# Kernel optimization log

Measured on AMD Instinct MI355X. Metric: run time of the kernel, lower is better.

The kernel has to match this reference:

```python
import jax, jax.numpy as jnp
import numpy as np

# Interpretation constants (external PersistentHomology class unavailable):
# each sample's feature vector is a point cloud of N_POINTS points in R^POINT_DIM.
N_POINTS = 1024
POINT_DIM = 128
WEIGHT = 1.0
N_TARGET_DIMS = 2  # target_dimensions = [0, 1]; H1 diagram is empty -> contributes 0


def _h0_mean_persistence(pts):
    """Exact H0 persistence of the Vietoris-Rips filtration of a point cloud.

    H0 pairs are (birth=0, death=w_e) for each edge w_e of the Euclidean MST,
    so persistence values are exactly the MST edge lengths (Prim's algorithm,
    vectorized over points, sequential over the N-1 tree-growth steps).
    pts: [N, d] -> scalar mean persistence.
    """
    n = pts.shape[0]
    mindist0 = jnp.linalg.norm(pts - pts[0], axis=-1)          # [N]
    visited0 = jnp.zeros((n,), dtype=bool).at[0].set(True)

    def step(carry, _):
        mindist, visited = carry
        masked = jnp.where(visited, jnp.inf, mindist)          # [N]
        j = jnp.argmin(masked)
        death = masked[j]                                      # MST edge length
        visited = visited.at[j].set(True)
        newd = jnp.linalg.norm(pts - pts[j], axis=-1)          # [N]
        mindist = jnp.minimum(mindist, newd)
        return (mindist, visited), death

    (_, _), deaths = jax.lax.scan(step, (mindist0, visited0), None, length=n - 1)
    return jnp.mean(deaths)


def setup_inputs() -> dict:
    key = jax.random.key(0)
    representations = jax.random.normal(key, (128, N_POINTS * POINT_DIM), dtype=jnp.float32)
    return {"representations": representations}


def reference(representations) -> jnp.ndarray:
    b = representations.shape[0]
    pts = representations.reshape(b, N_POINTS, POINT_DIM)      # per-sample point cloud
    per_sample = jax.vmap(_h0_mean_persistence)(pts)           # [B] mean H0 persistence
    # original: sum over batch and target dims (H1 empty), / (B * n_dims), * weight
    loss = jnp.sum(per_sample) / (b * N_TARGET_DIMS)
    return WEIGHT * loss
```

## Files before the change

kernel.cpp:

```cpp
#include <hip/hip_runtime.h>

typedef unsigned int uint_t;
typedef unsigned short ushort_t;
typedef unsigned char uchar_t;
typedef _Float16 h2 __attribute__((ext_vector_type(2)));
typedef _Float16 f16x8 __attribute__((ext_vector_type(8)));
typedef float f32x4 __attribute__((ext_vector_type(4)));

#define NPTS 1024
#define DIM  128
#define NH2  64

__device__ __forceinline__ float dot2f(uint_t a, uint_t b, float c) {
#if __has_builtin(__builtin_amdgcn_fdot2)
    return __builtin_amdgcn_fdot2(__builtin_bit_cast(h2, a),
                                  __builtin_bit_cast(h2, b), c, false);
#else
    h2 ha = __builtin_bit_cast(h2, a);
    h2 hb = __builtin_bit_cast(h2, b);
    c += (float)ha[0] * (float)hb[0];
    c += (float)ha[1] * (float)hb[1];
    return c;
#endif
}

__device__ __forceinline__ uint_t umin_u(uint_t a, uint_t b) { return a < b ? a : b; }
__device__ __forceinline__ uint_t umax_u(uint_t a, uint_t b) { return a > b ? a : b; }
__device__ __forceinline__ uint_t pk_min_u16(uint_t a, uint_t b) {
    uint_t d; asm("v_pk_min_u16 %0, %1, %2" : "=v"(d) : "v"(a), "v"(b)); return d;
}
__device__ __forceinline__ uint_t pk_max_u16(uint_t a, uint_t b) {
    uint_t d; asm("v_pk_max_u16 %0, %1, %2" : "=v"(d) : "v"(a), "v"(b)); return d;
}

#define DPP_UMIN(x, ctrl)                                                       \
    x = umin_u(x, (uint_t)__builtin_amdgcn_update_dpp((int)(x), (int)(x),       \
                                                      (ctrl), 0xf, 0xf, false))
#define DPP_REDUCE(x)                                                           \
    do { DPP_UMIN(x, 0x111); DPP_UMIN(x, 0x112); DPP_UMIN(x, 0x114);            \
         DPP_UMIN(x, 0x118); DPP_UMIN(x, 0x142); DPP_UMIN(x, 0x143); } while (0)

#define SEL_LO 0x05020400u
#define SEL_HI 0x07020600u

__device__ __forceinline__ void gload16(const void* g, void* l) {
#if __has_builtin(__builtin_amdgcn_global_load_lds)
    __builtin_amdgcn_global_load_lds(
        (__attribute__((address_space(1))) void*)(g),
        (__attribute__((address_space(3))) void*)(l), 16, 0, 0);
#else
    *(uint4*)l = *(const uint4*)g;
#endif
}

__global__ __launch_bounds__(256)
void prep_kernel(const float* __restrict__ reps, ushort_t* __restrict__ P16,
                 float* __restrict__ norms) {
    const int t   = threadIdx.x;
    const int row = blockIdx.x * 16 + (t >> 4);
    const int kx  = (t & 15) * 8;
    const float* src = reps + (size_t)row * DIM + kx;
    float4 v0 = *(const float4*)src;
    float4 v1 = *(const float4*)(src + 4);
    _Float16 h[8] = {(_Float16)v0.x, (_Float16)v0.y, (_Float16)v0.z, (_Float16)v0.w,
                     (_Float16)v1.x, (_Float16)v1.y, (_Float16)v1.z, (_Float16)v1.w};
    float nrm = 0.f;
    uint_t pk[4];
#pragma unroll
    for (int i = 0; i < 4; ++i) {
        float a = (float)h[2 * i], b = (float)h[2 * i + 1];
        nrm += a * a + b * b;
        pk[i] = (uint_t)__builtin_bit_cast(ushort_t, h[2 * i]) |
                ((uint_t)__builtin_bit_cast(ushort_t, h[2 * i + 1]) << 16);
    }
    *(uint4*)(P16 + (size_t)row * DIM + kx) = make_uint4(pk[0], pk[1], pk[2], pk[3]);
#pragma unroll
    for (int m = 1; m <= 8; m <<= 1) nrm += __shfl_xor(nrm, m, 16);
    if ((t & 15) == 0) norms[row] = nrm;
}

__global__ __launch_bounds__(256)
void norms_kernel(const float* __restrict__ reps, float* __restrict__ norms) {
    const int t   = threadIdx.x;
    const int row = blockIdx.x * 16 + (t >> 4);
    const int kx  = (t & 15) * 8;
    const float* src = reps + (size_t)row * DIM + kx;
    float4 v0 = *(const float4*)src;
    float4 v1 = *(const float4*)(src + 4);
    float nrm = 0.f;
    {
        _Float16 h[8] = {(_Float16)v0.x, (_Float16)v0.y, (_Float16)v0.z, (_Float16)v0.w,
                         (_Float16)v1.x, (_Float16)v1.y, (_Float16)v1.z, (_Float16)v1.w};
#pragma unroll
        for (int i = 0; i < 8; ++i) { float a = (float)h[i]; nrm += a * a; }
    }
#pragma unroll
    for (int m = 1; m <= 8; m <<= 1) nrm += __shfl_xor(nrm, m, 16);
    if ((t & 15) == 0) norms[row] = nrm;
}

__device__ __forceinline__ int swz(int row, int seg) {
    return (row << 7) + (((seg ^ row) & 15) << 3);
}
__device__ __forceinline__ uint_t packh2(float a, float b) {
    h2 p; p[0] = (_Float16)a; p[1] = (_Float16)b;
    return __builtin_bit_cast(uint_t, p);
}

__device__ __forceinline__ void gram_core_epilogue(
        f32x4 acc[2][8], const float* nrmS, uchar_t* Ds,
        int ti, int tj, int lane, int w) {
    const int cj = lane & 15;
    const int r4 = (lane >> 4) * 4;
    float na[2][4], nb[8];
#pragma unroll
    for (int mt = 0; mt < 2; ++mt)
#pragma unroll
        for (int r = 0; r < 4; ++r)
            na[mt][r] = nrmS[ti * 128 + w * 32 + mt * 16 + r4 + r];
#pragma unroll
    for (int nt = 0; nt < 8; ++nt) nb[nt] = nrmS[tj * 128 + nt * 16 + cj];
#pragma unroll
    for (int mt = 0; mt < 2; ++mt)
#pragma unroll
        for (int nt = 0; nt < 8; ++nt) {
            const int gj = tj * 128 + nt * 16 + cj;
#pragma unroll
            for (int r = 0; r < 4; ++r) {
                const int gi = ti * 128 + w * 32 + mt * 16 + r4 + r;
                float d2 = fmaxf(na[mt][r] + nb[nt] - 2.f * acc[mt][nt][r], 0.f);
                uint_t q = (uint_t)(d2 * 0.5f + 0.5f);
                q = q > 255u ? 255u : q;
                Ds[((size_t)gi << 10) + gj] = (uchar_t)q;
            }
        }
}

__global__ __launch_bounds__(256, 2)
void gram16_kernel(const ushort_t* __restrict__ P16, const float* __restrict__ norms,
                   uchar_t* __restrict__ D8, int xcd_affine) {
    __shared__ ushort_t At[128 * 128];
    __shared__ ushort_t Bt[128 * 128];
    const int bid = blockIdx.x;
    int s, tile;
    if (xcd_affine) {
        const int x = bid & 7, k = bid >> 3;
        s    = x + ((k >> 6) << 3);
        tile = k & 63;
    } else {
        s    = bid >> 6;
        tile = bid & 63;
    }
    const int ti = tile >> 3, tj = tile & 7;
    const int t  = threadIdx.x, lane = t & 63, w = t >> 6;

    const ushort_t* Pa = P16 + (((size_t)s * NPTS + (size_t)ti * 128) << 7);
    const ushort_t* Pb = P16 + (((size_t)s * NPTS + (size_t)tj * 128) << 7);
#pragma unroll
    for (int i = 0; i < 8; ++i) {
        const int c   = t + i * 256;
        const int row = c >> 4;
        const int seg = (c ^ row) & 15;
        const size_t go = ((size_t)row << 7) + (size_t)seg * 8;
        gload16(Pa + go, &At[(size_t)c * 8]);
        gload16(Pb + go, &Bt[(size_t)c * 8]);
    }
    __syncthreads();

    f32x4 acc[2][8] = {};
    const int mrow = lane & 15;
    const int lg   = lane >> 4;
#pragma unroll
    for (int q = 0; q < 4; ++q) {
        const int seg = q * 4 + lg;
        f16x8 a0 = *(const f16x8*)&At[swz(w * 32 + mrow, seg)];
        f16x8 a1 = *(const f16x8*)&At[swz(w * 32 + 16 + mrow, seg)];
#pragma unroll
        for (int nt = 0; nt < 8; ++nt) {
            f16x8 b = *(const f16x8*)&Bt[swz(nt * 16 + mrow, seg)];
            acc[0][nt] = __builtin_amdgcn_mfma_f32_16x16x32_f16(a0, b, acc[0][nt], 0, 0, 0);
            acc[1][nt] = __builtin_amdgcn_mfma_f32_16x16x32_f16(a1, b, acc[1][nt], 0, 0, 0);
        }
    }
    gram_core_epilogue(acc, norms + (size_t)s * NPTS, D8 + ((size_t)s << 20),
                       ti, tj, lane, w);
}

__global__ __launch_bounds__(256, 2)
void gram_kernel(const float* __restrict__ reps, const float* __restrict__ norms,
                 uchar_t* __restrict__ D8, int s_base) {
    __shared__ ushort_t At[128 * 128];
    __shared__ ushort_t Bt[128 * 128];
    const int bid  = blockIdx.x;
    const int sl   = bid >> 6, tile = bid & 63, ti = tile >> 3, tj = tile & 7;
    const int s    = s_base + sl;
    const int t    = threadIdx.x, lane = t & 63, w = t >> 6;

    const float* Pa = reps + ((size_t)s * NPTS + (size_t)ti * 128) * DIM;
    const float* Pb = reps + ((size_t)s * NPTS + (size_t)tj * 128) * DIM;
#pragma unroll
    for (int i = 0; i < 8; ++i) {
        int c = t + i * 256, row = c >> 4, seg = c & 15;
        const float* pa = Pa + row * DIM + seg * 8;
        const float* pb = Pb + row * DIM + seg * 8;
        float4 a0 = *(const float4*)pa, a1 = *(const float4*)(pa + 4);
        float4 b0 = *(const float4*)pb, b1 = *(const float4*)(pb + 4);
        *(uint4*)&At[swz(row, seg)] = make_uint4(packh2(a0.x, a0.y), packh2(a0.z, a0.w),
                                                 packh2(a1.x, a1.y), packh2(a1.z, a1.w));
        *(uint4*)&Bt[swz(row, seg)] = make_uint4(packh2(b0.x, b0.y), packh2(b0.z, b0.w),
                                                 packh2(b1.x, b1.y), packh2(b1.z, b1.w));
    }
    __syncthreads();

    f32x4 acc[2][8] = {};
    const int mrow = lane & 15;
    const int lg   = lane >> 4;
#pragma unroll
    for (int q = 0; q < 4; ++q) {
        const int seg = q * 4 + lg;
        f16x8 a0 = *(const f16x8*)&At[swz(w * 32 + mrow, seg)];
        f16x8 a1 = *(const f16x8*)&At[swz(w * 32 + 16 + mrow, seg)];
#pragma unroll
        for (int nt = 0; nt < 8; ++nt) {
            f16x8 b = *(const f16x8*)&Bt[swz(nt * 16 + mrow, seg)];
            acc[0][nt] = __builtin_amdgcn_mfma_f32_16x16x32_f16(a0, b, acc[0][nt], 0, 0, 0);
            acc[1][nt] = __builtin_amdgcn_mfma_f32_16x16x32_f16(a1, b, acc[1][nt], 0, 0, 0);
        }
    }
    gram_core_epilogue(acc, norms + (size_t)s * NPTS, D8 + ((size_t)sl << 20),
                       ti, tj, lane, w);
}

__global__ __launch_bounds__(256)
void nn4_kernel(const uchar_t* __restrict__ D8, uint_t* __restrict__ NN4) {
    const int lane = threadIdx.x & 63;
    const int wv   = threadIdx.x >> 6;
    const int base = blockIdx.x * 64 + wv * 16;

    uint_t slotv[8];
#pragma unroll
    for (int m = 0; m < 8; ++m)
        slotv[m] = ((uint_t)(2 * m + 1) << 16) | (uint_t)(2 * m);

    uint4 rc = ((const uint4*)(D8 + ((size_t)base << 10)))[lane];
    for (int i = 0; i < 16; ++i) {
        const int row = base + i;
        uint4 rn = rc;
        if (i < 15)
            rn = ((const uint4*)(D8 + ((size_t)(row + 1) << 10)))[lane];

        uint_t md[8];
        md[0] = __builtin_amdgcn_perm(rc.x, slotv[0], SEL_LO);
        md[1] = __builtin_amdgcn_perm(rc.x, slotv[1], SEL_HI);
        md[2] = __builtin_amdgcn_perm(rc.y, slotv[2], SEL_LO);
        md[3] = __builtin_amdgcn_perm(rc.y, slotv[3], SEL_HI);
        md[4] = __builtin_amdgcn_perm(rc.z, slotv[4], SEL_LO);
        md[5] = __builtin_amdgcn_perm(rc.z, slotv[5], SEL_HI);
        md[6] = __builtin_amdgcn_perm(rc.w, slotv[6], SEL_LO);
        md[7] = __builtin_amdgcn_perm(rc.w, slotv[7], SEL_HI);
        {
            const int r_in = row & 1023;
            const bool win = (r_in >> 4) == lane;
            const uint_t s4 = (uint_t)(r_in & 15);
#pragma unroll
            for (int m = 0; m < 8; ++m) {
                uint_t h = (win && s4 == 2u * m)      ? 0x0000FFFFu
                         : (win && s4 == 2u * m + 1u) ? 0xFFFF0000u : 0u;
                md[m] |= h;
            }
        }
        uint_t out4[4];
#pragma unroll
        for (int k = 0; k < 4; ++k) {
            uint_t t0 = pk_min_u16(pk_min_u16(md[0], md[1]), pk_min_u16(md[2], md[3]));
            uint_t t1 = pk_min_u16(pk_min_u16(md[4], md[5]), pk_min_u16(md[6], md[7]));
            uint_t tt = pk_min_u16(t0, t1);
            uint_t v16 = umin_u(tt & 0xFFFFu, tt >> 16);
            uint_t key = ((v16 & 0xFF00u) << 2) | ((uint_t)lane << 4) | (v16 & 15u);
            DPP_REDUCE(key);
            uint_t g = (uint_t)__builtin_amdgcn_readlane((int)key, 63);
            out4[k] = g;
            if (k < 3) {
                const uint_t wl = (g >> 4) & 63u, ws = g & 15u;
                const bool win = (uint_t)lane == wl;
#pragma unroll
                for (int m = 0; m < 8; ++m) {
                    uint_t h = (win && ws == 2u * m)      ? 0x0000FFFFu
                             : (win && ws == 2u * m + 1u) ? 0xFFFF0000u : 0u;
                    md[m] |= h;
                }
            }
        }
        if (lane == 0)
            *(uint4*)(NN4 + (size_t)row * 4) = make_uint4(out4[0], out4[1],
                                                          out4[2], out4[3]);
        rc = rn;
    }
}

__global__ __launch_bounds__(1024)
void boruvka4_kernel(const uchar_t* __restrict__ D8, const uint_t* __restrict__ NN4,
                     float* __restrict__ out, float scale) {
    const int sl   = blockIdx.x;
    const int v    = threadIdx.x;
    const int lane = v & 63;
    const int wv   = v >> 6;
    const uchar_t* Dbase = D8 + ((size_t)sl << 20);

    __shared__ ushort_t root16[NPTS];
    __shared__ uint_t   best[NPTS];
    __shared__ ushort_t rq[64];
    __shared__ uint_t   rqn, ncomp_s;
    __shared__ float    fsum[16];

    uint4 nA = *(const uint4*)(NN4 + (((size_t)sl << 10) + (size_t)v) * 4);
    uint_t nn[4] = {nA.x, nA.y, nA.z, nA.w};

    root16[v] = (ushort_t)v;
    float acc = 0.f;
    __syncthreads();

    for (int round = 0; round < 48; ++round) {
        best[v] = 0xFFFFFFFFu;
        if (v == 0) { rqn = 0; ncomp_s = 0; }
        __syncthreads();

        const uint_t rv = root16[v];

        uint_t cand = 0xFFFFFFFFu;
#pragma unroll
        for (int k = 0; k < 4; ++k) {
            uint_t e = nn[k];
            uint_t j = e & 1023u;
            if (root16[j] != (ushort_t)rv) {
                uint_t q = e >> 10;
                uint_t a = umin_u((uint_t)v, j), b = umax_u((uint_t)v, j);
                cand = umin_u(cand, (q << 20) | (a << 10) | b);
            }
        }
        if (cand != 0xFFFFFFFFu) atomicMin(&best[rv], cand);
        __syncthreads();

        if (rv == (uint_t)v && best[v] == 0xFFFFFFFFu) {
            uint_t idx = atomicAdd(&rqn, 1u);
            if (idx < 64u) rq[idx] = (ushort_t)v;
        }
        __syncthreads();

        if (rqn != 0u) {
            const uint_t nq = umin_u(rqn, 64u);
            for (uint_t qi = (uint_t)wv; qi < nq; qi += 16) {
                const uint_t row = rq[qi];
                const uint_t rr  = root16[row];
                uint4 r = ((const uint4*)(Dbase + ((size_t)row << 10)))[lane];
                uint_t bl = 0xFFFFFFFFu;
                const uint_t base = (uint_t)lane * 16u;
#pragma unroll
                for (int k = 0; k < 16; ++k) {
                    uint_t j = base + (uint_t)k;
                    uint_t q = (k < 4  ? (r.x >> (8 * k))
                              : k < 8  ? (r.y >> (8 * (k - 4)))
                              : k < 12 ? (r.z >> (8 * (k - 8)))
                                       : (r.w >> (8 * (k - 12)))) & 0xFFu;
                    uint_t a = umin_u(row, j), b = umax_u(row, j);
                    if (root16[j] != (ushort_t)rr)
                        bl = umin_u(bl, (q << 20) | (a << 10) | b);
                }
                DPP_REDUCE(bl);
                uint_t g = (uint_t)__builtin_amdgcn_readlane((int)bl, 63);
                if (lane == 0 && g != 0xFFFFFFFFu) atomicMin(&best[rr], g);
            }
            __syncthreads();
        }

        bool hook = false;
        uint_t o = (uint_t)v;
        if (rv == (uint_t)v) {
            uint_t K = best[v];
            if (K != 0xFFFFFFFFu) {
                uint_t a = (K >> 10) & 1023u, b = K & 1023u, q = K >> 20;
                uint_t ra = root16[a], rb = root16[b];
                o = (ra == (uint_t)v) ? rb : ra;
                if (o < (uint_t)v) {
                    hook = true;
                    acc += sqrtf(2.0f * (float)q);
                }
            }
        }
        __syncthreads();
        if (hook) root16[v] = (ushort_t)o;
        __syncthreads();

        uint_t r = root16[v];
        uint_t pr = root16[r];
        for (int sg = 0; sg < 64 && pr != r; ++sg) { r = pr; pr = root16[r]; }
        __syncthreads();
        root16[v] = (ushort_t)r;

        unsigned long long ball = __ballot(r == (uint_t)v);
        if (lane == 0) atomicAdd(&ncomp_s, (uint_t)__popcll(ball));
        __syncthreads();
        if (ncomp_s == 1u) break;
    }

#pragma unroll
    for (int m = 32; m >= 1; m >>= 1) acc += __shfl_xor(acc, m, 64);
    if (lane == 0) fsum[wv] = acc;
    __syncthreads();
    if (v == 0) {
        float s = 0.f;
#pragma unroll
        for (int i = 0; i < 16; ++i) s += fsum[i];
        atomicAdd(out, s * scale);
    }
}

__global__ __launch_bounds__(1024)
void boruvka_kernel(const uchar_t* __restrict__ D8, float* __restrict__ out,
                    float scale) {
    const int sl   = blockIdx.x;
    const int v    = threadIdx.x;
    const int lane = v & 63;
    const int wv   = v >> 6;
    const uchar_t* Dbase = D8 + ((size_t)sl << 20);

    __shared__ uint_t   nnlist[NPTS * 8];
    __shared__ ushort_t root16[NPTS];
    __shared__ uint_t   best[NPTS];
    __shared__ ushort_t rq[NPTS];
    __shared__ uint_t   rqn, ncomp_s;
    __shared__ float    fsum[16];

    uint_t slotv[8];
#pragma unroll
    for (int m = 0; m < 8; ++m)
        slotv[m] = ((uint_t)(2 * m + 1) << 16) | (uint_t)(2 * m);

    {
        uint4 rc = ((const uint4*)(Dbase + ((size_t)wv << 10)))[lane];
        for (int i = 0; i < 64; ++i) {
            const int row = wv + 16 * i;
            uint4 rn = rc;
            if (i < 63)
                rn = ((const uint4*)(Dbase + ((size_t)(row + 16) << 10)))[lane];
            uint_t md[8];
            md[0] = __builtin_amdgcn_perm(rc.x, slotv[0], SEL_LO);
            md[1] = __builtin_amdgcn_perm(rc.x, slotv[1], SEL_HI);
            md[2] = __builtin_amdgcn_perm(rc.y, slotv[2], SEL_LO);
            md[3] = __builtin_amdgcn_perm(rc.y, slotv[3], SEL_HI);
            md[4] = __builtin_amdgcn_perm(rc.z, slotv[4], SEL_LO);
            md[5] = __builtin_amdgcn_perm(rc.z, slotv[5], SEL_HI);
            md[6] = __builtin_amdgcn_perm(rc.w, slotv[6], SEL_LO);
            md[7] = __builtin_amdgcn_perm(rc.w, slotv[7], SEL_HI);
            {
                const bool win = (row >> 4) == lane;
                const uint_t s4 = (uint_t)(row & 15);
#pragma unroll
                for (int m = 0; m < 8; ++m) {
                    uint_t h = (win && s4 == 2u * m)      ? 0x0000FFFFu
                             : (win && s4 == 2u * m + 1u) ? 0xFFFF0000u : 0u;
                    md[m] |= h;
                }
            }
#pragma unroll
            for (int k = 0; k < 8; ++k) {
                uint_t t0 = pk_min_u16(pk_min_u16(md[0], md[1]), pk_min_u16(md[2], md[3]));
                uint_t t1 = pk_min_u16(pk_min_u16(md[4], md[5]), pk_min_u16(md[6], md[7]));
                uint_t tt = pk_min_u16(t0, t1);
                uint_t v16 = umin_u(tt & 0xFFFFu, tt >> 16);
                uint_t key = ((v16 & 0xFF00u) << 2) | ((uint_t)lane << 4) | (v16 & 15u);
                DPP_REDUCE(key);
                uint_t g = (uint_t)__builtin_amdgcn_readlane((int)key, 63);
                if (lane == 0) nnlist[row * 8 + k] = g;
                const uint_t wl = (g >> 4) & 63u, ws = g & 15u;
                const bool win = (uint_t)lane == wl;
#pragma unroll
                for (int m = 0; m < 8; ++m) {
                    uint_t h = (win && ws == 2u * m)      ? 0x0000FFFFu
                             : (win && ws == 2u * m + 1u) ? 0xFFFF0000u : 0u;
                    md[m] |= h;
                }
            }
            rc = rn;
        }
    }
    root16[v] = (ushort_t)v;
    __syncthreads();

    uint_t nn[8];
#pragma unroll
    for (int k = 0; k < 8; ++k) nn[k] = nnlist[v * 8 + k];
    const uint_t q8 = nn[7] >> 10;

    float acc = 0.f;
    for (int round = 0; round < 12; ++round) {
        best[v] = 0xFFFFFFFFu;
        if (v == 0) { rqn = 0; ncomp_s = 0; }
        __syncthreads();
        const uint_t rv = root16[v];
        uint_t cand = 0xFFFFFFFFu;
#pragma unroll
        for (int k = 0; k < 8; ++k) {
            uint_t e = nn[k];
            uint_t j = e & 1023u;
            if (root16[j] != (ushort_t)rv) {
                uint_t q = e >> 10;
                uint_t a = umin_u((uint_t)v, j), b = umax_u((uint_t)v, j);
                cand = umin_u(cand, (q << 20) | (a << 10) | b);
            }
        }
        if (cand != 0xFFFFFFFFu) atomicMin(&best[rv], cand);
        if (cand == 0xFFFFFFFFu || (cand >> 20) >= q8) {
            uint_t idx = atomicAdd(&rqn, 1u);
            rq[idx] = (ushort_t)v;
        }
        __syncthreads();
        for (uint_t qi = (uint_t)wv; qi < rqn; qi += 16) {
            const uint_t row = rq[qi];
            const uint_t rr  = root16[row];
            uint4 r = ((const uint4*)(Dbase + ((size_t)row << 10)))[lane];
            uint_t bl = 0xFFFFFFFFu;
            const uint_t base = (uint_t)lane * 16u;
#pragma unroll
            for (int k = 0; k < 16; ++k) {
                uint_t j = base + (uint_t)k;
                uint_t q = (k < 4  ? (r.x >> (8 * k))
                          : k < 8  ? (r.y >> (8 * (k - 4)))
                          : k < 12 ? (r.z >> (8 * (k - 8)))
                                   : (r.w >> (8 * (k - 12)))) & 0xFFu;
                uint_t a = umin_u(row, j), b = umax_u(row, j);
                if (root16[j] != (ushort_t)rr)
                    bl = umin_u(bl, (q << 20) | (a << 10) | b);
            }
            DPP_REDUCE(bl);
            uint_t g = (uint_t)__builtin_amdgcn_readlane((int)bl, 63);
            if (lane == 0 && g != 0xFFFFFFFFu) atomicMin(&best[rr], g);
        }
        __syncthreads();
        const bool isroot = (rv == (uint_t)v);
        bool hook = false;
        uint_t o = (uint_t)v;
        if (isroot) {
            uint_t K = best[v];
            if (K != 0xFFFFFFFFu) {
                uint_t a = (K >> 10) & 1023u, b = K & 1023u, q = K >> 20;
                uint_t ra = root16[a], rb = root16[b];
                o = (ra == (uint_t)v) ? rb : ra;
                bool mutual = (best[o] == K);
                if (!mutual || (uint_t)v > o) {
                    hook = true;
                    acc += sqrtf(2.0f * (float)q);
                }
            }
        }
        __syncthreads();
        if (hook) root16[v] = (ushort_t)o;
        __syncthreads();
        uint_t r = root16[v];
        uint_t pr = root16[r];
        for (int sgs = 0; sgs < 1024 && pr != r; ++sgs) { r = pr; pr = root16[r]; }
        __syncthreads();
        root16[v] = (ushort_t)r;
        unsigned long long ball = __ballot(r == (uint_t)v);
        if (lane == 0) atomicAdd(&ncomp_s, (uint_t)__popcll(ball));
        __syncthreads();
        if (ncomp_s == 1u) break;
    }
#pragma unroll
    for (int m = 32; m >= 1; m >>= 1) acc += __shfl_xor(acc, m, 64);
    if (lane == 0) fsum[wv] = acc;
    __syncthreads();
    if (v == 0) {
        float s = 0.f;
#pragma unroll
        for (int i = 0; i < 16; ++i) s += fsum[i];
        atomicAdd(out, s * scale);
    }
}

__global__ __launch_bounds__(64, 1)
void prim_u8_kernel(const uchar_t* __restrict__ D8, float* __restrict__ out,
                    float scale) {
    const int sl   = blockIdx.x;
    const int lane = threadIdx.x;
    const uchar_t* Dbase = D8 + ((size_t)sl << 20);

    uint_t md[8], po[8], slotv[8];
#pragma unroll
    for (int m = 0; m < 8; ++m) {
        md[m] = 0xFFFFFFFFu; po[m] = 0u;
        slotv[m] = ((uint_t)(2 * m + 1) << 16) | (uint_t)(2 * m);
    }
    const uint_t lane16 = (uint_t)lane << 4;
    uint_t p   = 0;
    float  acc = 0.f;

    for (int it = 0; it < NPTS - 1; ++it) {
        const uint4* rp = (const uint4*)(Dbase + ((size_t)p << 10));
        uint4 r = rp[lane];
        const bool  win = (p >> 4) == (uint_t)lane;
        const uint_t s4 = p & 15u;
#pragma unroll
        for (int m = 0; m < 8; ++m) {
            uint_t h = (win && s4 == 2u * m)      ? 0x0000FFFFu
                     : (win && s4 == 2u * m + 1u) ? 0xFFFF0000u : 0u;
            md[m] |= h; po[m] |= h;
        }
        md[0] = pk_min_u16(md[0], pk_max_u16(__builtin_amdgcn_perm(r.x, slotv[0], SEL_LO), po[0]));
        md[1] = pk_min_u16(md[1], pk_max_u16(__builtin_amdgcn_perm(r.x, slotv[1], SEL_HI), po[1]));
        md[2] = pk_min_u16(md[2], pk_max_u16(__builtin_amdgcn_perm(r.y, slotv[2], SEL_LO), po[2]));
        md[3] = pk_min_u16(md[3], pk_max_u16(__builtin_amdgcn_perm(r.y, slotv[3], SEL_HI), po[3]));
        md[4] = pk_min_u16(md[4], pk_max_u16(__builtin_amdgcn_perm(r.z, slotv[4], SEL_LO), po[4]));
        md[5] = pk_min_u16(md[5], pk_max_u16(__builtin_amdgcn_perm(r.z, slotv[5], SEL_HI), po[5]));
        md[6] = pk_min_u16(md[6], pk_max_u16(__builtin_amdgcn_perm(r.w, slotv[6], SEL_LO), po[6]));
        md[7] = pk_min_u16(md[7], pk_max_u16(__builtin_amdgcn_perm(r.w, slotv[7], SEL_HI), po[7]));

        uint_t t0 = pk_min_u16(pk_min_u16(md[0], md[1]), pk_min_u16(md[2], md[3]));
        uint_t t1 = pk_min_u16(pk_min_u16(md[4], md[5]), pk_min_u16(md[6], md[7]));
        uint_t tt = pk_min_u16(t0, t1);
        uint_t v16 = umin_u(tt & 0xFFFFu, tt >> 16);

        uint_t key = ((v16 & 0xFF00u) << 2) | lane16 | (v16 & 15u);
        DPP_REDUCE(key);
        uint_t g = (uint_t)__builtin_amdgcn_readlane((int)key, 63);

        p = g & 1023u;
        acc += sqrtf(2.0f * (float)(g >> 10));
    }
    if (lane == 0) atomicAdd(out, acc * scale);
}

#define NTHR 256
#define NWAVE 4
#define PPT  4
__global__ __launch_bounds__(NTHR, 1)
void prim_mst_kernel(const float* __restrict__ reps, float* __restrict__ out,
                     float scale) {
    const int s = blockIdx.x, t = threadIdx.x, lane = t & 63, wave = t >> 6;
    __shared__ uint4  sc[NH2 / 4];
    __shared__ float  snrm;
    __shared__ __align__(16) uint_t warr[NWAVE];
    __shared__ float  facc[NWAVE];
    uint_t cx[PPT][NH2]; float nrm[PPT], mind[PPT];
#pragma unroll
    for (int p = 0; p < PPT; ++p) {
        const float4* src = (const float4*)(reps + (size_t)s * (NPTS * DIM) +
                                            (size_t)(p * NTHR + t) * DIM);
        float n = 0.f;
#pragma unroll
        for (int k = 0; k < 32; ++k) {
            float4 v = src[k];
            h2 a; a[0] = (_Float16)v.x; a[1] = (_Float16)v.y;
            h2 b; b[0] = (_Float16)v.z; b[1] = (_Float16)v.w;
            cx[p][2 * k] = __builtin_bit_cast(uint_t, a);
            cx[p][2 * k + 1] = __builtin_bit_cast(uint_t, b);
            n = dot2f(cx[p][2 * k], cx[p][2 * k], n);
            n = dot2f(cx[p][2 * k + 1], cx[p][2 * k + 1], n);
        }
        nrm[p] = n; mind[p] = 3.0e38f;
    }
    uint_t vis = 0;
    if (t == 0) {
#pragma unroll
        for (int k = 0; k < NH2 / 4; ++k)
            sc[k] = make_uint4(cx[0][4 * k], cx[0][4 * k + 1], cx[0][4 * k + 2], cx[0][4 * k + 3]);
        snrm = nrm[0]; vis = 1;
    }
    __syncthreads();
    float acc = 0.f;
    for (int it = 0; it < NPTS - 1; ++it) {
        const float bn = snrm;
        float e0[PPT], e1[PPT];
#pragma unroll
        for (int p = 0; p < PPT; ++p) { e0[p] = 0.f; e1[p] = 0.f; }
#pragma unroll
        for (int k = 0; k < NH2 / 4; ++k) {
            uint4 q = sc[k];
#pragma unroll
            for (int p = 0; p < PPT; ++p) {
                e0[p] = dot2f(cx[p][4 * k + 0], q.x, e0[p]);
                e1[p] = dot2f(cx[p][4 * k + 1], q.y, e1[p]);
                e0[p] = dot2f(cx[p][4 * k + 2], q.z, e0[p]);
                e1[p] = dot2f(cx[p][4 * k + 3], q.w, e1[p]);
            }
        }
        uint_t key = 0xFFFFFFFFu;
#pragma unroll
        for (int p = 0; p < PPT; ++p) {
            float d2 = fmaxf(bn + nrm[p] - 2.f * (e0[p] + e1[p]), 0.f);
            mind[p] = fminf(mind[p], d2);
            uint_t kp = ((vis >> p) & 1u) ? 0xFFFFFFFFu
                      : ((__float_as_uint(mind[p]) & 0xFFFFFC00u) | (uint_t)(p * NTHR + t));
            key = umin_u(key, kp);
        }
        DPP_REDUCE(key);
        uint_t wkey = (uint_t)__builtin_amdgcn_readlane((int)key, 63);
        if (lane == 0) warr[wave] = wkey;
        __syncthreads();
        uint4 wv = *(const uint4*)warr;
        uint_t g = umin_u(umin_u(wv.x, wv.y), umin_u(wv.z, wv.w));
        const int j = (int)(g & 0x3FFu), jp = j >> 8;
        if ((j & (NTHR - 1)) == t) {
#pragma unroll
            for (int p = 0; p < PPT; ++p)
                if (jp == p) {
#pragma unroll
                    for (int k = 0; k < NH2 / 4; ++k)
                        sc[k] = make_uint4(cx[p][4 * k], cx[p][4 * k + 1],
                                           cx[p][4 * k + 2], cx[p][4 * k + 3]);
                    snrm = nrm[p]; acc += sqrtf(mind[p]);
                }
            vis |= 1u << jp;
        }
        __syncthreads();
    }
#pragma unroll
    for (int m = 32; m >= 1; m >>= 1) acc += __shfl_xor(acc, m, 64);
    if (lane == 0) facc[wave] = acc;
    __syncthreads();
    if (t == 0) atomicAdd(out, (facc[0] + facc[1] + facc[2] + facc[3]) * scale);
}

extern "C" void kernel_launch(void* const* d_in, const int* in_sizes, int n_in,
                              void* d_out, int out_size, void* d_ws, size_t ws_size,
                              hipStream_t stream) {
    const float* reps = (const float*)d_in[0];
    float*       out  = (float*)d_out;
    const int ns = in_sizes[0] / (NPTS * DIM);
    const float scale = 1.0f / ((float)(NPTS - 1) * (float)ns * 2.0f);

    hipMemsetAsync(out, 0, sizeof(float), stream);

    const size_t bytes_D  = (size_t)ns << 20;
    const size_t bytes_P  = (size_t)ns << 18;
    const size_t bytes_NN = (size_t)ns << 14;
    const size_t bytes_N  = (size_t)ns << 12;

    if (ws_size >= bytes_D + bytes_P + bytes_NN + bytes_N) {
        uchar_t*  D8    = (uchar_t*)d_ws;
        ushort_t* P16   = (ushort_t*)((char*)d_ws + bytes_D);
        uint_t*   NN4   = (uint_t*)((char*)d_ws + bytes_D + bytes_P);
        float*    norms = (float*)((char*)d_ws + bytes_D + bytes_P + bytes_NN);
        const int xcd_affine = ((ns & 7) == 0) ? 1 : 0;
        prep_kernel<<<dim3(ns * 64), dim3(256), 0, stream>>>(reps, P16, norms);
        gram16_kernel<<<dim3(ns * 64), dim3(256), 0, stream>>>(P16, norms, D8, xcd_affine);
        nn4_kernel<<<dim3(ns * 16), dim3(256), 0, stream>>>(D8, NN4);
        boruvka4_kernel<<<dim3(ns), dim3(1024), 0, stream>>>(D8, NN4, out, scale);
    } else if (ws_size >= bytes_D + bytes_N) {
        uchar_t* D8    = (uchar_t*)d_ws;
        float*   norms = (float*)((char*)d_ws + bytes_D);
        norms_kernel<<<dim3(ns * 64), dim3(256), 0, stream>>>(reps, norms);
        gram_kernel<<<dim3(ns * 64), dim3(256), 0, stream>>>(reps, norms, D8, 0);
        boruvka_kernel<<<dim3(ns), dim3(1024), 0, stream>>>(D8, out, scale);
    } else {
        int nc = 0;
        size_t norms_off = 0;
        if (ws_size > bytes_N + (1u << 20)) {
            norms_off = (ws_size - bytes_N) & ~(size_t)15;
            nc = (int)(norms_off >> 20);
            if (nc > ns) nc = ns;
        }
        if (nc >= 32) {
            uchar_t* D8    = (uchar_t*)d_ws;
            float*   norms = (float*)((char*)d_ws + norms_off);
            norms_kernel<<<dim3(ns * 64), dim3(256), 0, stream>>>(reps, norms);
            for (int base = 0; base < ns; base += nc) {
                const int n = (ns - base < nc) ? (ns - base) : nc;
                gram_kernel<<<dim3(n * 64), dim3(256), 0, stream>>>(reps, norms, D8, base);
                prim_u8_kernel<<<dim3(n), dim3(64), 0, stream>>>(D8, out, scale);
            }
        } else {
            prim_mst_kernel<<<dim3(ns), dim3(NTHR), 0, stream>>>(reps, out, scale);
        }
    }
}
```

Baseline: 250.2 us.

## Stream A operand from global into registers and pack epilogue stores via DPP

```diff
diff --git a/kernel.cpp b/kernel.cpp
--- a/kernel.cpp
+++ b/kernel.cpp
@@ -136,10 +136,9 @@
         }
 }
 
-__global__ __launch_bounds__(256, 2)
+__global__ __launch_bounds__(256, 4)
 void gram16_kernel(const ushort_t* __restrict__ P16, const float* __restrict__ norms,
                    uchar_t* __restrict__ D8, int xcd_affine) {
-    __shared__ ushort_t At[128 * 128];
     __shared__ ushort_t Bt[128 * 128];
     const int bid = blockIdx.x;
     int s, tile;
@@ -161,29 +160,75 @@
         const int c   = t + i * 256;
         const int row = c >> 4;
         const int seg = (c ^ row) & 15;
-        const size_t go = ((size_t)row << 7) + (size_t)seg * 8;
-        gload16(Pa + go, &At[(size_t)c * 8]);
-        gload16(Pb + go, &Bt[(size_t)c * 8]);
-    }
-    __syncthreads();
-
-    f32x4 acc[2][8] = {};
+        gload16(Pb + ((size_t)row << 7) + (size_t)seg * 8, &Bt[(size_t)c * 8]);
+    }
+
     const int mrow = lane & 15;
     const int lg   = lane >> 4;
+    const ushort_t* parow0 = Pa + ((w * 32 + mrow) << 7);
+    const ushort_t* parow1 = Pa + ((w * 32 + 16 + mrow) << 7);
+    f16x8 a0 = *(const f16x8*)(parow0 + lg * 8);
+    f16x8 a1 = *(const f16x8*)(parow1 + lg * 8);
+    __syncthreads();
+
+    f32x4 acc[2][8] = {};
 #pragma unroll
     for (int q = 0; q < 4; ++q) {
         const int seg = q * 4 + lg;
-        f16x8 a0 = *(const f16x8*)&At[swz(w * 32 + mrow, seg)];
-        f16x8 a1 = *(const f16x8*)&At[swz(w * 32 + 16 + mrow, seg)];
+        f16x8 a0c = a0, a1c = a1;
+        if (q < 3) {
+            a0 = *(const f16x8*)(parow0 + ((q + 1) * 4 + lg) * 8);
+            a1 = *(const f16x8*)(parow1 + ((q + 1) * 4 + lg) * 8);
+        }
 #pragma unroll
         for (int nt = 0; nt < 8; ++nt) {
             f16x8 b = *(const f16x8*)&Bt[swz(nt * 16 + mrow, seg)];
-            acc[0][nt] = __builtin_amdgcn_mfma_f32_16x16x32_f16(a0, b, acc[0][nt], 0, 0, 0);
-            acc[1][nt] = __builtin_amdgcn_mfma_f32_16x16x32_f16(a1, b, acc[1][nt], 0, 0, 0);
-        }
-    }
-    gram_core_epilogue(acc, norms + (size_t)s * NPTS, D8 + ((size_t)s << 20),
-                       ti, tj, lane, w);
+            acc[0][nt] = __builtin_amdgcn_mfma_f32_16x16x32_f16(a0c, b, acc[0][nt], 0, 0, 0);
+            acc[1][nt] = __builtin_amdgcn_mfma_f32_16x16x32_f16(a1c, b, acc[1][nt], 0, 0, 0);
+        }
+    }
+
+    const float* nrmS = norms + (size_t)s * NPTS;
+    uchar_t*     Ds   = D8 + ((size_t)s << 20);
+    const int cj = lane & 15;
+    const int r4 = (lane >> 4) * 4;
+    float ha[2][4], hb[8];
+#pragma unroll
+    for (int mt = 0; mt < 2; ++mt)
+#pragma unroll
+        for (int r = 0; r < 4; ++r)
+            ha[mt][r] = 0.5f * nrmS[ti * 128 + w * 32 + mt * 16 + r4 + r] + 0.5f;
+#pragma unroll
+    for (int nt = 0; nt < 8; ++nt) hb[nt] = 0.5f * nrmS[tj * 128 + nt * 16 + cj];
+
+    const uint_t rr    = (uint_t)(lane & 3);
+    const uint_t sel01 = rr | ((rr + 4u) << 8);
+    uchar_t* rowbase = Ds + (((size_t)(ti * 128 + w * 32 + r4 + (int)rr)) << 10)
+                          + tj * 128 + (lane & 12);
+#pragma unroll
+    for (int mt = 0; mt < 2; ++mt)
+#pragma unroll
+        for (int nt = 0; nt < 8; ++nt) {
+            uint_t cp = 0;
+#pragma unroll
+            for (int r = 0; r < 4; ++r) {
+                float f = (ha[mt][r] + hb[nt]) - acc[mt][nt][r];
+#if __has_builtin(__builtin_amdgcn_cvt_pk_u8_f32)
+                cp = __builtin_amdgcn_cvt_pk_u8_f32(f, (uint_t)r, cp);
+#else
+                uint_t qb = (uint_t)fminf(fmaxf(f, 0.f), 255.f);
+                cp |= qb << (8 * r);
+#endif
+            }
+            uint_t d0 = (uint_t)__builtin_amdgcn_update_dpp((int)cp, (int)cp, 0x00, 0xf, 0xf, false);
+            uint_t d1 = (uint_t)__builtin_amdgcn_update_dpp((int)cp, (int)cp, 0x55, 0xf, 0xf, false);
+            uint_t d2 = (uint_t)__builtin_amdgcn_update_dpp((int)cp, (int)cp, 0xaa, 0xf, 0xf, false);
+            uint_t d3 = (uint_t)__builtin_amdgcn_update_dpp((int)cp, (int)cp, 0xff, 0xf, 0xf, false);
+            uint_t lo  = __builtin_amdgcn_perm(d1, d0, sel01);
+            uint_t hi  = __builtin_amdgcn_perm(d3, d2, sel01);
+            uint_t res = __builtin_amdgcn_perm(hi, lo, 0x05040100u);
+            *(uint_t*)(rowbase + mt * (16 << 10) + nt * 16) = res;
+        }
 }
 
 __global__ __launch_bounds__(256, 2)
```

Measured after the change: 244.8 us. -2.2%, faster.
